# Kernel optimization log

Hardware: AMD Instinct MI355X
Metric: run time of the kernel (lower is better)

Reference implementation:

```python
import jax, jax.numpy as jnp
import numpy as np

D_MODEL = 1024
BS, K = 16, 64


def setup_inputs() -> dict:
    key = jax.random.key(0)
    k1, k2 = jax.random.split(key)
    Mp_cls = jax.random.normal(k1, (BS, K, D_MODEL), dtype=jnp.float32)
    mask_p = jnp.ones((BS, K, 4, K), dtype=bool)  # unused (no rnk_transformer)
    # nn.Linear(4*d_model, 3, bias=False) weight: [3, 4*d_model]
    W = jax.random.normal(k2, (3, 4 * D_MODEL), dtype=jnp.float32) * (4 * D_MODEL) ** -0.5
    return {"Mp_cls": Mp_cls, "mask_p": mask_p, "W": W}


def reference(Mp_cls, mask_p, W):
    # Pairwise scores: feature at [b,i,j] = cat(A[b,j], A[b,i], |A[b,j]-A[b,i]|, A[b,i]*A[b,j])
    # scores = feature @ W.T  -> [bs,K,K,3]. We split W into its 4 d_model blocks
    # so the concatenated [bs,K,K,4d] tensor is never materialized.
    d = Mp_cls.shape[-1]
    W1, W2, W3, W4 = W[:, :d], W[:, d:2 * d], W[:, 2 * d:3 * d], W[:, 3 * d:]
    t1 = jnp.einsum('bjd,cd->bjc', Mp_cls, W1)[:, None, :, :]          # from unsqueeze(1).expand
    t2 = jnp.einsum('bid,cd->bic', Mp_cls, W2)[:, :, None, :]          # from unsqueeze(2).expand
    diff = jnp.abs(Mp_cls[:, None, :, :] - Mp_cls[:, :, None, :])      # [bs,K,K,d]
    t3 = jnp.einsum('bijd,cd->bijc', diff, W3)
    t4 = jnp.einsum('bid,bjd,cd->bijc', Mp_cls, Mp_cls, W4)            # elementwise product term
    return t1 + t2 + t3 + t4  # [bs, K, K, 3]
```

## Files before the change

### kernel.cpp

```cpp
#include <hip/hip_runtime.h>

#define D_MODEL 1024
#define KK 64
#define BSZ 16

#define MPT2_F4_PER_B (256 * 64)
#define PPART_OFF (BSZ * 256 * 64 * 4)

__global__ __launch_bounds__(256) void prep2(
    const float* __restrict__ Mp, const float* __restrict__ W,
    float* __restrict__ MpT2, float* __restrict__ Ppart)
{
    __shared__ float tile[64 * 65];
    __shared__ float Wt[6 * 64];
    __shared__ float part[64][6][4];

    const int b  = blockIdx.x;
    const int dt = blockIdx.y;
    const int t  = threadIdx.x;
    const int d0 = dt * 64;

    const float* __restrict__ src = Mp + (size_t)b * KK * D_MODEL;
#pragma unroll
    for (int p = 0; p < 4; ++p) {
        const int idx = p * 256 + t;
        const int j   = idx >> 4;
        const int c4  = (idx & 15) * 4;
        const float4 v = *reinterpret_cast<const float4*>(src + j * D_MODEL + d0 + c4);
        float* dst = &tile[j * 65 + c4];
        dst[0] = v.x; dst[1] = v.y; dst[2] = v.z; dst[3] = v.w;
    }
    for (int u = t; u < 384; u += 256) {
        const int cc = u >> 6, d = u & 63;
        Wt[cc * 64 + d] = W[(cc < 3 ? cc : cc - 3) * 4096 + (cc < 3 ? 0 : 1024) + d0 + d];
    }
    __syncthreads();

    float4* __restrict__ dstb =
        reinterpret_cast<float4*>(MpT2) + (size_t)b * MPT2_F4_PER_B + (d0 >> 2) * 64;
#pragma unroll
    for (int p = 0; p < 4; ++p) {
        const int idx = p * 256 + t;
        const int d4l = idx >> 6;
        const int j   = idx & 63;
        const float* s = &tile[j * 65 + d4l * 4];
        float4 v; v.x = s[0]; v.y = s[1]; v.z = s[2]; v.w = s[3];
        dstb[d4l * 64 + j] = v;
    }

    {
        const int j = t >> 2, q = t & 3;
        float s[6] = {0.f, 0.f, 0.f, 0.f, 0.f, 0.f};
#pragma unroll
        for (int dd = 0; dd < 16; ++dd) {
            const int d   = q * 16 + dd;
            const float m = tile[j * 65 + d];
#pragma unroll
            for (int cc = 0; cc < 6; ++cc) s[cc] = fmaf(m, Wt[cc * 64 + d], s[cc]);
        }
#pragma unroll
        for (int cc = 0; cc < 6; ++cc) part[j][cc][q] = s[cc];
    }
    __syncthreads();

    for (int u = t; u < 384; u += 256) {
        const int j = u / 6, cc = u % 6;
        const float v = part[j][cc][0] + part[j][cc][1] + part[j][cc][2] + part[j][cc][3];
        Ppart[((size_t)(b * 16 + dt) * 64 + j) * 6 + cc] = v;
    }
}

__global__ __launch_bounds__(256) void pair2(
    const float* __restrict__ Mp, const float* __restrict__ W,
    const float* __restrict__ MpT2, const float* __restrict__ Ppart,
    float* __restrict__ out)
{
    __shared__ float red[4][2][3][64];

    const int b    = blockIdx.x;
    const int i0   = blockIdx.y * 2;
    const int lane = threadIdx.x & 63;
    const int wid  = threadIdx.x >> 6;
    const int uwid = __builtin_amdgcn_readfirstlane(wid);

    const float4* __restrict__ mjp =
        reinterpret_cast<const float4*>(MpT2) + (size_t)b * MPT2_F4_PER_B + uwid * 64 * 64 + lane;
    const float* __restrict__ mi0p = Mp + ((size_t)(b * KK + i0)) * D_MODEL + uwid * 256;
    const float* __restrict__ mi1p = mi0p + D_MODEL;
    const float* __restrict__ w3b  = W + 2048 + uwid * 256;
    const float* __restrict__ w4b  = W + 3072 + uwid * 256;

    float a00 = 0.f, a01 = 0.f, a02 = 0.f;
    float a10 = 0.f, a11 = 0.f, a12 = 0.f;

#pragma unroll 4
    for (int k4 = 0; k4 < 64; ++k4) {
        const float4 mj = mjp[k4 * 64];
        const float4 m0 = *reinterpret_cast<const float4*>(mi0p + k4 * 4);
        const float4 m1 = *reinterpret_cast<const float4*>(mi1p + k4 * 4);
        const float4 u0 = *reinterpret_cast<const float4*>(w3b + k4 * 4);
        const float4 u1 = *reinterpret_cast<const float4*>(w3b + 4096 + k4 * 4);
        const float4 u2 = *reinterpret_cast<const float4*>(w3b + 8192 + k4 * 4);
        const float4 v0 = *reinterpret_cast<const float4*>(w4b + k4 * 4);
        const float4 v1 = *reinterpret_cast<const float4*>(w4b + 4096 + k4 * 4);
        const float4 v2 = *reinterpret_cast<const float4*>(w4b + 8192 + k4 * 4);

#define EL(E) {                                                        \
        const float df0 = fabsf(m0.E - mj.E), pr0 = m0.E * mj.E;       \
        a00 = fmaf(df0, u0.E, a00);  a00 = fmaf(pr0, v0.E, a00);       \
        a01 = fmaf(df0, u1.E, a01);  a01 = fmaf(pr0, v1.E, a01);       \
        a02 = fmaf(df0, u2.E, a02);  a02 = fmaf(pr0, v2.E, a02);       \
        const float df1 = fabsf(m1.E - mj.E), pr1 = m1.E * mj.E;       \
        a10 = fmaf(df1, u0.E, a10);  a10 = fmaf(pr1, v0.E, a10);       \
        a11 = fmaf(df1, u1.E, a11);  a11 = fmaf(pr1, v1.E, a11);       \
        a12 = fmaf(df1, u2.E, a12);  a12 = fmaf(pr1, v2.E, a12); }
        EL(x) EL(y) EL(z) EL(w)
#undef EL
    }

    red[wid][0][0][lane] = a00;  red[wid][0][1][lane] = a01;  red[wid][0][2][lane] = a02;
    red[wid][1][0][lane] = a10;  red[wid][1][1][lane] = a11;  red[wid][1][2][lane] = a12;
    __syncthreads();

    if (wid < 2) {
        const int i = i0 + wid;
        const float* __restrict__ Pb = Ppart + (size_t)b * 16 * 64 * 6;
        float p1[3] = {0.f, 0.f, 0.f}, p2[3] = {0.f, 0.f, 0.f};
#pragma unroll
        for (int dt = 0; dt < 16; ++dt) {
            const float* q1 = Pb + (dt * 64 + lane) * 6;
            const float* q2 = Pb + (dt * 64 + i) * 6 + 3;
#pragma unroll
            for (int c = 0; c < 3; ++c) { p1[c] += q1[c]; p2[c] += q2[c]; }
        }
        float* __restrict__ orow = out + (((size_t)(b * KK + i)) * KK + lane) * 3;
#pragma unroll
        for (int c = 0; c < 3; ++c) {
            orow[c] = red[0][wid][c][lane] + red[1][wid][c][lane]
                    + red[2][wid][c][lane] + red[3][wid][c][lane]
                    + p1[c] + p2[c];
        }
    }
}

extern "C" void kernel_launch(void* const* d_in, const int* in_sizes, int n_in,
                              void* d_out, int out_size, void* d_ws, size_t ws_size,
                              hipStream_t stream)
{
    const float* Mp = (const float*)d_in[0];
    const float* W  = (const float*)d_in[2];
    float* out = (float*)d_out;

    float* MpT2  = (float*)d_ws;
    float* Ppart = MpT2 + PPART_OFF;

    prep2<<<dim3(BSZ, 16), 256, 0, stream>>>(Mp, W, MpT2, Ppart);
    pair2<<<dim3(BSZ, 32), 256, 0, stream>>>(Mp, W, MpT2, Ppart, out);
}
```

Before: 100.9 us.

## Stage W and i-rows in LDS, compute four rows per block with eight waves

The pair kernel now stages the W3/W4 weights and four query rows of Mp into shared memory, then has eight waves each cover 128 features for four i-rows. Each MpT2 load is reused across four rows instead of two, and the grid shrinks to 16x16 blocks of 512 threads. The Ppart layout is changed to channel-major so the final reads coalesce across lanes. In exchange the kernel uses more LDS and more accumulator registers, and launches half as many blocks, which may lower occupancy.

```diff
diff --git a/kernel.cpp b/kernel.cpp
--- a/kernel.cpp
+++ b/kernel.cpp
@@ -64,81 +64,106 @@
     __syncthreads();
 
     for (int u = t; u < 384; u += 256) {
-        const int j = u / 6, cc = u % 6;
+        const int cc = u >> 6, j = u & 63;
         const float v = part[j][cc][0] + part[j][cc][1] + part[j][cc][2] + part[j][cc][3];
-        Ppart[((size_t)(b * 16 + dt) * 64 + j) * 6 + cc] = v;
+        Ppart[((size_t)(b * 16 + dt) * 6 + cc) * 64 + j] = v;
     }
 }
 
-__global__ __launch_bounds__(256) void pair2(
+__global__ __launch_bounds__(512) void pair3(
     const float* __restrict__ Mp, const float* __restrict__ W,
     const float* __restrict__ MpT2, const float* __restrict__ Ppart,
     float* __restrict__ out)
 {
-    __shared__ float red[4][2][3][64];
+    __shared__ float Wlds[6 * 1024];
+    __shared__ float Milds[4 * 1024];
+    __shared__ float red[8][4][3][64];
 
     const int b    = blockIdx.x;
-    const int i0   = blockIdx.y * 2;
-    const int lane = threadIdx.x & 63;
-    const int wid  = threadIdx.x >> 6;
+    const int i0   = blockIdx.y * 4;
+    const int t    = threadIdx.x;
+    const int lane = t & 63;
+    const int wid  = t >> 6;
     const int uwid = __builtin_amdgcn_readfirstlane(wid);
 
-    const float4* __restrict__ mjp =
-        reinterpret_cast<const float4*>(MpT2) + (size_t)b * MPT2_F4_PER_B + uwid * 64 * 64 + lane;
-    const float* __restrict__ mi0p = Mp + ((size_t)(b * KK + i0)) * D_MODEL + uwid * 256;
-    const float* __restrict__ mi1p = mi0p + D_MODEL;
-    const float* __restrict__ w3b  = W + 2048 + uwid * 256;
-    const float* __restrict__ w4b  = W + 3072 + uwid * 256;
+    for (int u = t; u < 1536; u += 512) {
+        const int cc = u >> 8;
+        const int d4 = u & 255;
+        const float4 v = *reinterpret_cast<const float4*>(
+            W + (cc < 3 ? cc : cc - 3) * 4096 + (cc < 3 ? 2048 : 3072) + d4 * 4);
+        *reinterpret_cast<float4*>(&Wlds[cc * 1024 + d4 * 4]) = v;
+    }
+    for (int u = t; u < 1024; u += 512) {
+        const int r  = u >> 8;
+        const int d4 = u & 255;
+        const float4 v = *reinterpret_cast<const float4*>(
+            Mp + ((size_t)(b * KK + i0 + r)) * D_MODEL + d4 * 4);
+        *reinterpret_cast<float4*>(&Milds[r * 1024 + d4 * 4]) = v;
+    }
+    __syncthreads();
 
-    float a00 = 0.f, a01 = 0.f, a02 = 0.f;
-    float a10 = 0.f, a11 = 0.f, a12 = 0.f;
+    const float4* __restrict__ mjp = reinterpret_cast<const float4*>(MpT2)
+        + (size_t)b * MPT2_F4_PER_B + uwid * 32 * 64 + lane;
+    const int db = uwid * 128;
+
+    float a0c0 = 0.f, a0c1 = 0.f, a0c2 = 0.f;
+    float a1c0 = 0.f, a1c1 = 0.f, a1c2 = 0.f;
+    float a2c0 = 0.f, a2c1 = 0.f, a2c2 = 0.f;
+    float a3c0 = 0.f, a3c1 = 0.f, a3c2 = 0.f;
 
 #pragma unroll 4
-    for (int k4 = 0; k4 < 64; ++k4) {
+    for (int k4 = 0; k4 < 32; ++k4) {
         const float4 mj = mjp[k4 * 64];
-        const float4 m0 = *reinterpret_cast<const float4*>(mi0p + k4 * 4);
-        const float4 m1 = *reinterpret_cast<const float4*>(mi1p + k4 * 4);
-        const float4 u0 = *reinterpret_cast<const float4*>(w3b + k4 * 4);
-        const float4 u1 = *reinterpret_cast<const float4*>(w3b + 4096 + k4 * 4);
-        const float4 u2 = *reinterpret_cast<const float4*>(w3b + 8192 + k4 * 4);
-        const float4 v0 = *reinterpret_cast<const float4*>(w4b + k4 * 4);
-        const float4 v1 = *reinterpret_cast<const float4*>(w4b + 4096 + k4 * 4);
-        const float4 v2 = *reinterpret_cast<const float4*>(w4b + 8192 + k4 * 4);
+        const int dd = db + k4 * 4;
+        const float4 m0 = *reinterpret_cast<const float4*>(&Milds[dd]);
+        const float4 m1 = *reinterpret_cast<const float4*>(&Milds[1024 + dd]);
+        const float4 m2 = *reinterpret_cast<const float4*>(&Milds[2048 + dd]);
+        const float4 m3 = *reinterpret_cast<const float4*>(&Milds[3072 + dd]);
+        const float4 u0 = *reinterpret_cast<const float4*>(&Wlds[dd]);
+        const float4 u1 = *reinterpret_cast<const float4*>(&Wlds[1024 + dd]);
+        const float4 u2 = *reinterpret_cast<const float4*>(&Wlds[2048 + dd]);
+        const float4 v0 = *reinterpret_cast<const float4*>(&Wlds[3072 + dd]);
+        const float4 v1 = *reinterpret_cast<const float4*>(&Wlds[4096 + dd]);
+        const float4 v2 = *reinterpret_cast<const float4*>(&Wlds[5120 + dd]);
 
-#define EL(E) {                                                        \
-        const float df0 = fabsf(m0.E - mj.E), pr0 = m0.E * mj.E;       \
-        a00 = fmaf(df0, u0.E, a00);  a00 = fmaf(pr0, v0.E, a00);       \
-        a01 = fmaf(df0, u1.E, a01);  a01 = fmaf(pr0, v1.E, a01);       \
-        a02 = fmaf(df0, u2.E, a02);  a02 = fmaf(pr0, v2.E, a02);       \
-        const float df1 = fabsf(m1.E - mj.E), pr1 = m1.E * mj.E;       \
-        a10 = fmaf(df1, u0.E, a10);  a10 = fmaf(pr1, v0.E, a10);       \
-        a11 = fmaf(df1, u1.E, a11);  a11 = fmaf(pr1, v1.E, a11);       \
-        a12 = fmaf(df1, u2.E, a12);  a12 = fmaf(pr1, v2.E, a12); }
-        EL(x) EL(y) EL(z) EL(w)
-#undef EL
+#define ROWE(M, A0, A1, A2, E) {                                   \
+        const float df = fabsf(M.E - mj.E);                        \
+        const float pr = M.E * mj.E;                               \
+        A0 = fmaf(df, u0.E, A0);  A0 = fmaf(pr, v0.E, A0);         \
+        A1 = fmaf(df, u1.E, A1);  A1 = fmaf(pr, v1.E, A1);         \
+        A2 = fmaf(df, u2.E, A2);  A2 = fmaf(pr, v2.E, A2); }
+#define ALLR(E) ROWE(m0, a0c0, a0c1, a0c2, E) ROWE(m1, a1c0, a1c1, a1c2, E) \
+                ROWE(m2, a2c0, a2c1, a2c2, E) ROWE(m3, a3c0, a3c1, a3c2, E)
+        ALLR(x) ALLR(y) ALLR(z) ALLR(w)
+#undef ALLR
+#undef ROWE
     }
 
-    red[wid][0][0][lane] = a00;  red[wid][0][1][lane] = a01;  red[wid][0][2][lane] = a02;
-    red[wid][1][0][lane] = a10;  red[wid][1][1][lane] = a11;  red[wid][1][2][lane] = a12;
+    red[wid][0][0][lane] = a0c0; red[wid][0][1][lane] = a0c1; red[wid][0][2][lane] = a0c2;
+    red[wid][1][0][lane] = a1c0; red[wid][1][1][lane] = a1c1; red[wid][1][2][lane] = a1c2;
+    red[wid][2][0][lane] = a2c0; red[wid][2][1][lane] = a2c1; red[wid][2][2][lane] = a2c2;
+    red[wid][3][0][lane] = a3c0; red[wid][3][1][lane] = a3c1; red[wid][3][2][lane] = a3c2;
     __syncthreads();
 
-    if (wid < 2) {
+    if (wid < 4) {
         const int i = i0 + wid;
-        const float* __restrict__ Pb = Ppart + (size_t)b * 16 * 64 * 6;
-        float p1[3] = {0.f, 0.f, 0.f}, p2[3] = {0.f, 0.f, 0.f};
+        const float* __restrict__ Pb = Ppart + (size_t)b * 16 * 6 * 64;
+        float p[3] = {0.f, 0.f, 0.f};
 #pragma unroll
         for (int dt = 0; dt < 16; ++dt) {
-            const float* q1 = Pb + (dt * 64 + lane) * 6;
-            const float* q2 = Pb + (dt * 64 + i) * 6 + 3;
 #pragma unroll
-            for (int c = 0; c < 3; ++c) { p1[c] += q1[c]; p2[c] += q2[c]; }
+            for (int c = 0; c < 3; ++c) {
+                p[c] += Pb[(dt * 6 + c) * 64 + lane];
+                p[c] += Pb[(dt * 6 + 3 + c) * 64 + i];
+            }
         }
         float* __restrict__ orow = out + (((size_t)(b * KK + i)) * KK + lane) * 3;
 #pragma unroll
         for (int c = 0; c < 3; ++c) {
-            orow[c] = red[0][wid][c][lane] + red[1][wid][c][lane]
-                    + red[2][wid][c][lane] + red[3][wid][c][lane]
-                    + p1[c] + p2[c];
+            float s = p[c];
+#pragma unroll
+            for (int w = 0; w < 8; ++w) s += red[w][wid][c][lane];
+            orow[c] = s;
         }
     }
 }
@@ -155,5 +180,5 @@
     float* Ppart = MpT2 + PPART_OFF;
 
     prep2<<<dim3(BSZ, 16), 256, 0, stream>>>(Mp, W, MpT2, Ppart);
-    pair2<<<dim3(BSZ, 32), 256, 0, stream>>>(Mp, W, MpT2, Ppart, out);
+    pair3<<<dim3(BSZ, 16), 512, 0, stream>>>(Mp, W, MpT2, Ppart, out);
 }
```

Result: faster. 83.37 us (-17.3%).
